# Optimization experiments

Hardware: AMD Instinct MI355X
Metric: run time of the kernel (lower is better)

The kernel has to match this reference:

```python
import jax, jax.numpy as jnp
import numpy as np

B, T, D, H, FF, E = 4, 1024, 1024, 16, 4096, 8
HD = D // H
EPS = 1e-5


def layernorm(x, g, b):
    mu = jnp.mean(x, axis=-1, keepdims=True)
    var = jnp.mean(jnp.square(x - mu), axis=-1, keepdims=True)
    return (x - mu) * jax.lax.rsqrt(var + EPS) * g + b


def setup_inputs() -> dict:
    key = jax.random.key(0)
    ks = jax.random.split(key, 24)
    s = 0.02
    inp = {
        "src": jax.random.normal(ks[0], (B, T, D), jnp.float32),
        "frac": jax.random.uniform(ks[1], (B, T), jnp.float32),
        "Wq": jax.random.normal(ks[2], (D, D), jnp.float32) * s,
        "bq": jnp.zeros((D,), jnp.float32),
        "Wk": jax.random.normal(ks[3], (D, D), jnp.float32) * s,
        "bk": jnp.zeros((D,), jnp.float32),
        "Wv": jax.random.normal(ks[4], (D, D), jnp.float32) * s,
        "bv": jnp.zeros((D,), jnp.float32),
        "Wo": jax.random.normal(ks[5], (D, D), jnp.float32) * s,
        "bo": jnp.zeros((D,), jnp.float32),
        "alpha_pos": jax.random.normal(ks[6], (H,), jnp.float32) * s,
        "alpha_neg": jax.random.normal(ks[7], (H,), jnp.float32) * s,
        "gate_W": jax.random.normal(ks[8], (D, E), jnp.float32) * s,
        "gate_b": jnp.zeros((E,), jnp.float32),
        "W1": jax.random.normal(ks[9], (E, D, FF), jnp.float32) * s,
        "b1": jnp.zeros((E, FF), jnp.float32),
        "W2": jax.random.normal(ks[10], (E, FF, D), jnp.float32) * s,
        "b2": jnp.zeros((E, D), jnp.float32),
        "ln1_g": jnp.ones((D,), jnp.float32),
        "ln1_b": jnp.zeros((D,), jnp.float32),
        "ln2_g": jnp.ones((D,), jnp.float32),
        "ln2_b": jnp.zeros((D,), jnp.float32),
    }
    return inp


def reference(src, frac, Wq, bq, Wk, bk, Wv, bv, Wo, bo, alpha_pos, alpha_neg,
              gate_W, gate_b, W1, b1, W2, b2, ln1_g, ln1_b, ln2_g, ln2_b):
    # ---- attention with per-head stoichiometric bias ----
    q = (src @ Wq + bq).reshape(B, T, H, HD).transpose(0, 2, 1, 3)  # [B,H,T,hd]
    k = (src @ Wk + bk).reshape(B, T, H, HD).transpose(0, 2, 1, 3)
    v = (src @ Wv + bv).reshape(B, T, H, HD).transpose(0, 2, 1, 3)
    scale = HD ** -0.5
    scores = jnp.einsum('bhqd,bhkd->bhqk', q, k) * scale  # [B,H,T,T]
    Dm = frac[:, None, :] - frac[:, :, None]  # frac_j - frac_i, [B,T,T]
    bias = (alpha_pos[None, :, None, None] * jax.nn.relu(Dm)[:, None]
            - alpha_neg[None, :, None, None] * jax.nn.relu(-Dm)[:, None])
    probs = jax.nn.softmax(scores + bias, axis=-1)
    attn = jnp.einsum('bhqk,bhkd->bhqd', probs, v)
    attn = attn.transpose(0, 2, 1, 3).reshape(B, T, D) @ Wo + bo

    x = layernorm(src + attn, ln1_g, ln1_b)

    # ---- top-2 MoE FFN ----
    logits = x @ gate_W + gate_b  # [B,T,E]
    gscores = jax.nn.softmax(logits, axis=-1)
    top2_scores, top2_idx = jax.lax.top_k(gscores, 2)  # [B,T,2]
    # dense per-expert combine weight: score if expert in top-2 else 0
    weights = jnp.sum(jax.nn.one_hot(top2_idx, E, dtype=x.dtype)
                      * top2_scores[..., None], axis=-2)  # [B,T,E]
    ff = jnp.zeros_like(x)
    for e in range(E):  # small fixed expert count
        h = jax.nn.relu(x @ W1[e] + b1[e])
        ff = ff + weights[..., e:e + 1] * (h @ W2[e] + b2[e])

    return layernorm(x + ff, ln2_g, ln2_b)
```

## Files before the change

### kernel.cpp

```cpp
#include <hip/hip_runtime.h>
#include <stdint.h>

typedef unsigned short u16;
typedef unsigned int   u32;

using bf16x8 = __attribute__((ext_vector_type(8))) short;
using f32x4  = __attribute__((ext_vector_type(4))) float;

#define N_T   1024
#define N_D   1024
#define N_E   8
#define N_BT  4096
#define LNEPS 1e-5f

__device__ __forceinline__ u32 rne2(float a, float b) {
  u32 ua = __float_as_uint(a); ua = (ua + 0x7fffu + ((ua >> 16) & 1u)) >> 16;
  u32 ub = __float_as_uint(b); ub = (ub + 0x7fffu + ((ub >> 16) & 1u)) >> 16;
  return ua | (ub << 16);
}
__device__ __forceinline__ u16 rne1(float a) {
  u32 ua = __float_as_uint(a);
  return (u16)((ua + 0x7fffu + ((ua >> 16) & 1u)) >> 16);
}
__device__ __forceinline__ float bfhi_f(float a) {
  u32 ua = __float_as_uint(a);
  ua = (ua + 0x7fffu + ((ua >> 16) & 1u)) & 0xffff0000u;
  return __uint_as_float(ua);
}
__device__ __forceinline__ int fch(int row) { return (row & 3) ^ ((row >> 2) & 3); }
__device__ __forceinline__ int swz(int row, int chunk) {
  return row * 32 + (((chunk ^ fch(row)) & 3) << 3);
}
__device__ __forceinline__ float wred(float v) {
  #pragma unroll
  for (int o2 = 32; o2 > 0; o2 >>= 1) v += __shfl_xor(v, o2, 64);
  return v;
}
__device__ __forceinline__ f32x4 mfma16(bf16x8 a, bf16x8 b, f32x4 c) {
  return __builtin_amdgcn_mfma_f32_16x16x32_bf16(a, b, c, 0, 0, 0);
}
typedef __attribute__((address_space(1))) const u32 gas_u32;
typedef __attribute__((address_space(3))) u32 las_u32;
__device__ __forceinline__ void gl16(const void* g, void* l) {
  __builtin_amdgcn_global_load_lds((gas_u32*)g, (las_u32*)l, 16, 0, 0);
}

template<int SPLIT>
__global__ __launch_bounds__(256)
void transpose_bf16(const float* __restrict__ in, u16* __restrict__ outh,
                    u16* __restrict__ outl, int R, int C, float scale)
{
  __shared__ u16 th[64][68];
  __shared__ u16 tl[SPLIT ? 64 : 1][SPLIT ? 68 : 1];
  const long long zb = (long long)blockIdx.z * R * C;
  const float* srcp = in + zb;
  const int r0 = blockIdx.y * 64, c0 = blockIdx.x * 64;
  const int t = threadIdx.x;
  {
    const int rr = t >> 4, cc = (t & 15) << 2;
    #pragma unroll
    for (int i = 0; i < 4; i++) {
      const int r = rr + i * 16;
      float4 v = *(const float4*)(srcp + (long long)(r0 + r) * C + c0 + cc);
      v.x *= scale; v.y *= scale; v.z *= scale; v.w *= scale;
      if constexpr (SPLIT) {
        float hx = bfhi_f(v.x), hy = bfhi_f(v.y), hz = bfhi_f(v.z), hw = bfhi_f(v.w);
        *(uint2*)&th[r][cc] = make_uint2(rne2(hx, hy), rne2(hz, hw));
        *(uint2*)&tl[r][cc] = make_uint2(rne2(v.x - hx, v.y - hy), rne2(v.z - hz, v.w - hw));
      } else {
        *(uint2*)&th[r][cc] = make_uint2(rne2(v.x, v.y), rne2(v.z, v.w));
      }
    }
  }
  __syncthreads();
  {
    const int c = t >> 2, rs = (t & 3) << 4;
    const long long ob = zb + (long long)(c0 + c) * R + r0 + rs;
    u32 w[8];
    #pragma unroll
    for (int i = 0; i < 8; i++)
      w[i] = (u32)th[rs + 2*i][c] | ((u32)th[rs + 2*i + 1][c] << 16);
    *(uint4*)(outh + ob)     = make_uint4(w[0], w[1], w[2], w[3]);
    *(uint4*)(outh + ob + 8) = make_uint4(w[4], w[5], w[6], w[7]);
    if constexpr (SPLIT) {
      #pragma unroll
      for (int i = 0; i < 8; i++)
        w[i] = (u32)tl[rs + 2*i][c] | ((u32)tl[rs + 2*i + 1][c] << 16);
      *(uint4*)(outl + ob)     = make_uint4(w[0], w[1], w[2], w[3]);
      *(uint4*)(outl + ob + 8) = make_uint4(w[4], w[5], w[6], w[7]);
    }
  }
}

__global__ __launch_bounds__(256)
void trans4(const float* __restrict__ Wq, const float* __restrict__ Wk,
            const float* __restrict__ Wv, const float* __restrict__ Wo,
            u16* __restrict__ Bcath, u16* __restrict__ Bcatl,
            u16* __restrict__ WoTh, u16* __restrict__ WoTl)
{
  __shared__ u16 th[64][68];
  __shared__ u16 tl[64][68];
  const int z = blockIdx.z;
  const float* in = (z == 0) ? Wq : (z == 1) ? Wk : (z == 2) ? Wv : Wo;
  u16* outh = (z == 3) ? WoTh : (Bcath + (long long)z * 1024 * 1024);
  u16* outl = (z == 3) ? WoTl : (Bcatl + (long long)z * 1024 * 1024);
  const float scale = (z == 0) ? 0.125f : 1.0f;
  const int r0 = blockIdx.y * 64, c0 = blockIdx.x * 64;
  const int t = threadIdx.x;
  {
    const int rr = t >> 4, cc = (t & 15) << 2;
    #pragma unroll
    for (int i = 0; i < 4; i++) {
      const int r = rr + i * 16;
      float4 v = *(const float4*)(in + (long long)(r0 + r) * 1024 + c0 + cc);
      v.x *= scale; v.y *= scale; v.z *= scale; v.w *= scale;
      float hx = bfhi_f(v.x), hy = bfhi_f(v.y), hz = bfhi_f(v.z), hw = bfhi_f(v.w);
      *(uint2*)&th[r][cc] = make_uint2(rne2(hx, hy), rne2(hz, hw));
      *(uint2*)&tl[r][cc] = make_uint2(rne2(v.x - hx, v.y - hy), rne2(v.z - hz, v.w - hw));
    }
  }
  __syncthreads();
  {
    const int c = t >> 2, rs = (t & 3) << 4;
    const long long ob = (long long)(c0 + c) * 1024 + r0 + rs;
    u32 w[8];
    #pragma unroll
    for (int i = 0; i < 8; i++)
      w[i] = (u32)th[rs + 2*i][c] | ((u32)th[rs + 2*i + 1][c] << 16);
    *(uint4*)(outh + ob)     = make_uint4(w[0], w[1], w[2], w[3]);
    *(uint4*)(outh + ob + 8) = make_uint4(w[4], w[5], w[6], w[7]);
    #pragma unroll
    for (int i = 0; i < 8; i++)
      w[i] = (u32)tl[rs + 2*i][c] | ((u32)tl[rs + 2*i + 1][c] << 16);
    *(uint4*)(outl + ob)     = make_uint4(w[0], w[1], w[2], w[3]);
    *(uint4*)(outl + ob + 8) = make_uint4(w[4], w[5], w[6], w[7]);
  }
}

__global__ __launch_bounds__(256)
void bias_cat(const float* __restrict__ bq, const float* __restrict__ bk,
              const float* __restrict__ bv, float* __restrict__ bcat)
{
  const int i = blockIdx.x * 256 + threadIdx.x;
  if (i < 1024)       bcat[i] = bq[i] * 0.125f;
  else if (i < 2048)  bcat[i] = bk[i - 1024];
  else if (i < 3072)  bcat[i] = bv[i - 2048];
}

__global__ __launch_bounds__(256)
void vtrans_bf16(const u16* __restrict__ Vh, const u16* __restrict__ Vl, int ldv,
                 u16* __restrict__ Vth, u16* __restrict__ Vtl)
{
  __shared__ u16 th[64][72];
  __shared__ u16 tl[64][72];
  const int bh = blockIdx.y, b = bh >> 4, h = bh & 15;
  const int kt = blockIdx.x, tid = threadIdx.x;
  {
    const int sr = tid >> 2, scb = (tid & 3) << 4;
    const long long off = (long long)(b * N_T + kt * 64 + sr) * ldv + h * 64 + scb;
    const uint4* vh = (const uint4*)(Vh + off);
    const uint4* vl = (const uint4*)(Vl + off);
    *(uint4*)&th[sr][scb]     = vh[0];
    *(uint4*)&th[sr][scb + 8] = vh[1];
    *(uint4*)&tl[sr][scb]     = vl[0];
    *(uint4*)&tl[sr][scb + 8] = vl[1];
  }
  __syncthreads();
  {
    const int od = tid >> 2, os0 = (tid & 3) << 4;
    u16 wh[16], wl[16];
    #pragma unroll
    for (int i = 0; i < 16; i++) { wh[i] = th[os0 + i][od]; wl[i] = tl[os0 + i][od]; }
    u16* oph = Vth + (long long)(bh * 64 + od) * N_T + kt * 64 + os0;
    u16* opl = Vtl + (long long)(bh * 64 + od) * N_T + kt * 64 + os0;
    *(uint4*)oph = make_uint4((u32)wh[0] | ((u32)wh[1] << 16), (u32)wh[2] | ((u32)wh[3] << 16),
                              (u32)wh[4] | ((u32)wh[5] << 16), (u32)wh[6] | ((u32)wh[7] << 16));
    *(uint4*)(oph + 8) = make_uint4((u32)wh[8] | ((u32)wh[9] << 16), (u32)wh[10] | ((u32)wh[11] << 16),
                                    (u32)wh[12] | ((u32)wh[13] << 16), (u32)wh[14] | ((u32)wh[15] << 16));
    *(uint4*)opl = make_uint4((u32)wl[0] | ((u32)wl[1] << 16), (u32)wl[2] | ((u32)wl[3] << 16),
                              (u32)wl[4] | ((u32)wl[5] << 16), (u32)wl[6] | ((u32)wl[7] << 16));
    *(uint4*)(opl + 8) = make_uint4((u32)wl[8] | ((u32)wl[9] << 16), (u32)wl[10] | ((u32)wl[11] << 16),
                                    (u32)wl[12] | ((u32)wl[13] << 16), (u32)wl[14] | ((u32)wl[15] << 16));
  }
}

template<int ASPLIT, int GATHER, int DORELU, int DOSCALE, int OBF, int GROUPED, int CG>
__global__ __launch_bounds__(256, 2)
void gemm128(const void* __restrict__ Ap, int lda,
             const u16* __restrict__ Bhp, const u16* __restrict__ Blp,
             long long bstride,
             void* __restrict__ Cp, int ldc,
             const float* __restrict__ biasp, int bias_stride,
             const float* __restrict__ slot_wp,
             const int* __restrict__ tokidx,
             const int2* __restrict__ tilesp, const int* __restrict__ ntilesp,
             int Ksz, void* __restrict__ Cp2, float cscale)
{
  const int gx = gridDim.x, nwg = gx * gridDim.y;
  const int orig = blockIdx.y * gx + blockIdx.x;
  const int flat = (orig & 7) * (nwg >> 3) + (orig >> 3);
  const int cgsz = gx * CG;
  const int colg = flat / cgsz, rem = flat % cgsz;
  const int bxx = rem / CG;
  const int byy = colg * CG + rem % CG;

  int e = 0, row0;
  if constexpr (GROUPED) {
    if (bxx >= *ntilesp) return;
    const int2 dsc = tilesp[bxx];
    e = dsc.x; row0 = dsc.y;
  } else {
    row0 = bxx * 128;
  }
  const int col0 = byy * 128;

  __shared__ __align__(16) u16 AhS[ASPLIT ? 1 : 3][128 * 32];
  __shared__ __align__(16) u16 BhS[ASPLIT ? 1 : 3][128 * 32];
  __shared__ __align__(16) u16 AlS[ASPLIT ? 128 * 32 : 8];
  __shared__ __align__(16) u16 BlS[ASPLIT ? 128 * 32 : 8];

  const int tid = threadIdx.x, wid = tid >> 6, lane = tid & 63;
  const int wm = (wid >> 1) << 6, wn = (wid & 1) << 6;
  const int l15 = lane & 15, l4 = lane >> 4;

  const int srow0 = wid * 32 + (lane >> 2);
  const int srow1 = srow0 + 16;
  const int sg0 = ((lane & 3) ^ fch(srow0)) << 3;
  const int sg1 = ((lane & 3) ^ fch(srow1)) << 3;
  const int lo0 = wid * 1024, lo1 = wid * 1024 + 512;

  const u16* Bg0 = Bhp + (long long)e * bstride + (long long)(col0 + srow0) * Ksz + sg0;
  const u16* Bg1 = Bhp + (long long)e * bstride + (long long)(col0 + srow1) * Ksz + sg1;
  const u16* Blg0 = nullptr; const u16* Blg1 = nullptr;
  if constexpr (ASPLIT) {
    Blg0 = Blp + (long long)e * bstride + (long long)(col0 + srow0) * Ksz + sg0;
    Blg1 = Blp + (long long)e * bstride + (long long)(col0 + srow1) * Ksz + sg1;
  }

  const u16* Ag0 = nullptr; const u16* Ag1 = nullptr;
  if constexpr (!ASPLIT) {
    long long ar0, ar1;
    if constexpr (GATHER) { ar0 = tokidx[row0 + srow0]; ar1 = tokidx[row0 + srow1]; }
    else                  { ar0 = row0 + srow0;          ar1 = row0 + srow1; }
    Ag0 = (const u16*)Ap + ar0 * (long long)lda + sg0;
    Ag1 = (const u16*)Ap + ar1 * (long long)lda + sg1;
  }

  f32x4 acc[4][4] = {};
  const int nk = Ksz >> 5;

  if constexpr (!ASPLIT) {
    gl16(Ag0, &AhS[0][lo0]); gl16(Ag1, &AhS[0][lo1]);
    gl16(Bg0, &BhS[0][lo0]); gl16(Bg1, &BhS[0][lo1]);
    gl16(Ag0 + 32, &AhS[1][lo0]); gl16(Ag1 + 32, &AhS[1][lo1]);
    gl16(Bg0 + 32, &BhS[1][lo0]); gl16(Bg1 + 32, &BhS[1][lo1]);
    for (int kt = 0; kt < nk; kt++) {
      if (kt + 1 < nk) asm volatile("s_waitcnt vmcnt(4)" ::: "memory");
      else             asm volatile("s_waitcnt vmcnt(0)" ::: "memory");
      __syncthreads();
      const int bi = kt % 3;
      bf16x8 ah[4], bh[4];
      #pragma unroll
      for (int i = 0; i < 4; i++) {
        ah[i] = *(const bf16x8*)&AhS[bi][swz(wm + i * 16 + l15, l4)];
        bh[i] = *(const bf16x8*)&BhS[bi][swz(wn + i * 16 + l15, l4)];
      }
      #pragma unroll
      for (int i = 0; i < 4; i++)
        #pragma unroll
        for (int j = 0; j < 4; j++)
          acc[i][j] = mfma16(ah[i], bh[j], acc[i][j]);
      __syncthreads();
      if (kt + 2 < nk) {
        const int ko = (kt + 2) << 5;
        const int bn = (kt + 2) % 3;
        gl16(Ag0 + ko, &AhS[bn][lo0]);
        gl16(Ag1 + ko, &AhS[bn][lo1]);
        gl16(Bg0 + ko, &BhS[bn][lo0]);
        gl16(Bg1 + ko, &BhS[bn][lo1]);
      }
    }
  } else {
    const int prr = tid >> 1, pc2 = (tid & 1) << 1;
    const float* Arow = (const float*)Ap + (long long)(row0 + prr) * lda;
    uint4 sah0, sah1, sal0, sal1;
    auto gloadA = [&](int k0) {
      const float4* ap = (const float4*)(Arow + k0 + pc2 * 8);
      float4 f0 = ap[0], f1 = ap[1], f2 = ap[2], f3 = ap[3];
      float h0 = bfhi_f(f0.x), h1 = bfhi_f(f0.y), h2 = bfhi_f(f0.z), h3 = bfhi_f(f0.w);
      float h4 = bfhi_f(f1.x), h5 = bfhi_f(f1.y), h6 = bfhi_f(f1.z), h7 = bfhi_f(f1.w);
      sah0 = make_uint4(rne2(h0, h1), rne2(h2, h3), rne2(h4, h5), rne2(h6, h7));
      sal0 = make_uint4(rne2(f0.x - h0, f0.y - h1), rne2(f0.z - h2, f0.w - h3),
                        rne2(f1.x - h4, f1.y - h5), rne2(f1.z - h6, f1.w - h7));
      h0 = bfhi_f(f2.x); h1 = bfhi_f(f2.y); h2 = bfhi_f(f2.z); h3 = bfhi_f(f2.w);
      h4 = bfhi_f(f3.x); h5 = bfhi_f(f3.y); h6 = bfhi_f(f3.z); h7 = bfhi_f(f3.w);
      sah1 = make_uint4(rne2(h0, h1), rne2(h2, h3), rne2(h4, h5), rne2(h6, h7));
      sal1 = make_uint4(rne2(f2.x - h0, f2.y - h1), rne2(f2.z - h2, f2.w - h3),
                        rne2(f3.x - h4, f3.y - h5), rne2(f3.z - h6, f3.w - h7));
    };
    gloadA(0);
    for (int kt = 0; kt < nk; kt++) {
      __syncthreads();
      const int ko = kt << 5;
      *(uint4*)&AhS[0][swz(prr, pc2)]     = sah0;
      *(uint4*)&AhS[0][swz(prr, pc2 + 1)] = sah1;
      *(uint4*)&AlS[swz(prr, pc2)]        = sal0;
      *(uint4*)&AlS[swz(prr, pc2 + 1)]    = sal1;
      gl16(Bg0 + ko, &BhS[0][lo0]);
      gl16(Bg1 + ko, &BhS[0][lo1]);
      gl16(Blg0 + ko, &BlS[lo0]);
      gl16(Blg1 + ko, &BlS[lo1]);
      asm volatile("s_waitcnt vmcnt(0)" ::: "memory");
      __syncthreads();
      if (kt + 1 < nk) gloadA((kt + 1) << 5);

      bf16x8 ah[4], bh[4], al[4], bl[4];
      #pragma unroll
      for (int i = 0; i < 4; i++) {
        const int ar = wm + i * 16 + l15;
        const int br = wn + i * 16 + l15;
        ah[i] = *(const bf16x8*)&AhS[0][swz(ar, l4)];
        bh[i] = *(const bf16x8*)&BhS[0][swz(br, l4)];
        al[i] = *(const bf16x8*)&AlS[swz(ar, l4)];
        bl[i] = *(const bf16x8*)&BlS[swz(br, l4)];
      }
      #pragma unroll
      for (int i = 0; i < 4; i++) {
        #pragma unroll
        for (int j = 0; j < 4; j++) {
          acc[i][j] = mfma16(ah[i], bh[j], acc[i][j]);
          acc[i][j] = mfma16(ah[i], bl[j], acc[i][j]);
          acc[i][j] = mfma16(al[i], bh[j], acc[i][j]);
        }
      }
    }
  }

  #pragma unroll
  for (int i = 0; i < 4; i++) {
    #pragma unroll
    for (int j = 0; j < 4; j++) {
      const int orow0 = row0 + wm + i * 16 + (l4 << 2);
      const int ocol  = col0 + wn + j * 16 + l15;
      const float bv = biasp[(long long)e * bias_stride + col0 + wn + j * 16 + l15];
      #pragma unroll
      for (int q = 0; q < 4; q++) {
        float v = acc[i][j][q] + bv;
        if constexpr (DORELU) v = fmaxf(v, 0.f);
        const long long orow = orow0 + q;
        if constexpr (DOSCALE) v *= slot_wp[orow];
        if constexpr (OBF == 2) {
          const float vs = v * cscale;
          const float hi = bfhi_f(vs);
          ((u16*)Cp )[orow * ldc + ocol] = (u16)(__float_as_uint(hi) >> 16);
          ((u16*)Cp2)[orow * ldc + ocol] = rne1(vs - hi);
        } else if constexpr (OBF == 1) {
          ((u16*)Cp)[orow * ldc + ocol] = rne1(v);
        } else {
          ((float*)Cp)[orow * ldc + ocol] = v;
        }
      }
    }
  }
}

__global__ __launch_bounds__(256, 2)
void attn_mfma(const u16* __restrict__ Qh, const u16* __restrict__ Ql,
               const u16* __restrict__ Kh, const u16* __restrict__ Kl, int ldq,
               const u16* __restrict__ Vth, const u16* __restrict__ Vtl,
               const float* __restrict__ frac,
               const float* __restrict__ apos, const float* __restrict__ aneg,
               float* __restrict__ ctx)
{
  __shared__ __align__(16) u16 KhS[64 * 64];
  __shared__ __align__(16) u16 KlS[64 * 64];
  __shared__ __align__(16) u16 VhS[64 * 64];
  __shared__ __align__(16) u16 VlS[64 * 64];
  __shared__ __align__(16) u16 PS[4][32][72];
  __shared__ __align__(16) float fjS[64];

  const int bh = blockIdx.x, b = bh >> 4, h = bh & 15;
  const int tid = threadIdx.x, wid = tid >> 6, lane = tid & 63;
  const int l15 = lane & 15, l4 = lane >> 4;
  const int q0 = blockIdx.y * 128 + wid * 32;

  bf16x8 qh[2][2], ql[2][2];
  #pragma unroll
  for (int ni = 0; ni < 2; ni++) {
    const long long qoff = (long long)(b * N_T + q0 + ni * 16 + l15) * ldq + h * 64 + l4 * 8;
    #pragma unroll
    for (int ks = 0; ks < 2; ks++) {
      qh[ni][ks] = *(const bf16x8*)(Qh + qoff + ks * 32);
      ql[ni][ks] = *(const bf16x8*)(Ql + qoff + ks * 32);
    }
  }
  float fq[2];
  #pragma unroll
  for (int ni = 0; ni < 2; ni++) fq[ni] = frac[b * N_T + q0 + ni * 16 + l15];
  const float ap = apos[h], an = aneg[h];

  f32x4 acc[4][2] = {};
  float mrun[2] = {-3.0e38f, -3.0e38f}, lrun[2] = {0.f, 0.f};

  const int sr = tid >> 2, scb = (tid & 3) << 4;
  const int ch0 = ((scb >> 3) ^ (sr & 7)) << 3;
  const int ch1 = (((scb >> 3) + 1) ^ (sr & 7)) << 3;

  for (int kt = 0; kt < 16; kt++) {
    __syncthreads();
    {
      const long long koff = (long long)(b * N_T + kt * 64 + sr) * ldq + h * 64 + scb;
      const uint4* khp = (const uint4*)(Kh + koff);
      const uint4* klp = (const uint4*)(Kl + koff);
      const long long voff = (long long)(bh * 64 + sr) * N_T + kt * 64 + scb;
      const uint4* vhp = (const uint4*)(Vth + voff);
      const uint4* vlp = (const uint4*)(Vtl + voff);
      *(uint4*)&KhS[sr * 64 + ch0] = khp[0];
      *(uint4*)&KhS[sr * 64 + ch1] = khp[1];
      *(uint4*)&KlS[sr * 64 + ch0] = klp[0];
      *(uint4*)&KlS[sr * 64 + ch1] = klp[1];
      *(uint4*)&VhS[sr * 64 + ch0] = vhp[0];
      *(uint4*)&VhS[sr * 64 + ch1] = vhp[1];
      *(uint4*)&VlS[sr * 64 + ch0] = vlp[0];
      *(uint4*)&VlS[sr * 64 + ch1] = vlp[1];
    }
    if (tid < 64) fjS[tid] = frac[b * N_T + kt * 64 + tid];
    __syncthreads();

    f32x4 s[4][2] = {};
    #pragma unroll
    for (int ks = 0; ks < 2; ks++) {
      bf16x8 kh[4], kl[4];
      #pragma unroll
      for (int mj = 0; mj < 4; mj++) {
        const int row = mj * 16 + l15;
        const int ch = (((ks << 2) + l4) ^ (row & 7)) << 3;
        kh[mj] = *(const bf16x8*)&KhS[row * 64 + ch];
        kl[mj] = *(const bf16x8*)&KlS[row * 64 + ch];
      }
      #pragma unroll
      for (int mj = 0; mj < 4; mj++) {
        #pragma unroll
        for (int ni = 0; ni < 2; ni++) {
          s[mj][ni] = mfma16(kh[mj], qh[ni][ks], s[mj][ni]);
          s[mj][ni] = mfma16(kh[mj], ql[ni][ks], s[mj][ni]);
          s[mj][ni] = mfma16(kl[mj], qh[ni][ks], s[mj][ni]);
        }
      }
    }

    #pragma unroll
    for (int mj = 0; mj < 4; mj++) {
      const int kvb = mj * 16 + l4 * 4;
      const float f0 = fjS[kvb], f1 = fjS[kvb + 1], f2 = fjS[kvb + 2], f3 = fjS[kvb + 3];
      #pragma unroll
      for (int ni = 0; ni < 2; ni++) {
        float d0 = f0 - fq[ni], d1 = f1 - fq[ni], d2 = f2 - fq[ni], d3 = f3 - fq[ni];
        s[mj][ni][0] += (d0 > 0.f ? ap : an) * d0;
        s[mj][ni][1] += (d1 > 0.f ? ap : an) * d1;
        s[mj][ni][2] += (d2 > 0.f ? ap : an) * d2;
        s[mj][ni][3] += (d3 > 0.f ? ap : an) * d3;
      }
    }

    #pragma unroll
    for (int ni = 0; ni < 2; ni++) {
      float tm = s[0][ni][0];
      #pragma unroll
      for (int mj = 0; mj < 4; mj++) {
        tm = fmaxf(tm, fmaxf(fmaxf(s[mj][ni][0], s[mj][ni][1]),
                             fmaxf(s[mj][ni][2], s[mj][ni][3])));
      }
      tm = fmaxf(tm, __shfl_xor(tm, 16, 64));
      tm = fmaxf(tm, __shfl_xor(tm, 32, 64));
      const float nm = fmaxf(mrun[ni], tm);
      const float cor = __expf(mrun[ni] - nm);
      mrun[ni] = nm;
      lrun[ni] *= cor;
      #pragma unroll
      for (int md = 0; md < 4; md++) {
        acc[md][ni][0] *= cor; acc[md][ni][1] *= cor;
        acc[md][ni][2] *= cor; acc[md][ni][3] *= cor;
      }
      float rsum = 0.f;
      #pragma unroll
      for (int mj = 0; mj < 4; mj++) {
        #pragma unroll
        for (int r = 0; r < 4; r++) {
          const float p = __expf(s[mj][ni][r] - nm);
          s[mj][ni][r] = p;
          rsum += p;
        }
      }
      rsum += __shfl_xor(rsum, 16, 64);
      rsum += __shfl_xor(rsum, 32, 64);
      lrun[ni] += rsum;
    }

    #pragma unroll
    for (int ni = 0; ni < 2; ni++) {
      #pragma unroll
      for (int mj = 0; mj < 4; mj++) {
        float h0 = bfhi_f(s[mj][ni][0]), h1 = bfhi_f(s[mj][ni][1]);
        float h2 = bfhi_f(s[mj][ni][2]), h3 = bfhi_f(s[mj][ni][3]);
        u32* dst = (u32*)&PS[wid][ni * 16 + l15][mj * 16 + l4 * 4];
        dst[0] = rne2(h0, h1); dst[1] = rne2(h2, h3);
      }
    }
    bf16x8 pbh[2][2];
    #pragma unroll
    for (int ni = 0; ni < 2; ni++)
      #pragma unroll
      for (int ks = 0; ks < 2; ks++)
        pbh[ni][ks] = *(const bf16x8*)&PS[wid][ni * 16 + l15][ks * 32 + l4 * 8];

    #pragma unroll
    for (int ni = 0; ni < 2; ni++) {
      #pragma unroll
      for (int mj = 0; mj < 4; mj++) {
        float p0 = s[mj][ni][0], p1 = s[mj][ni][1], p2 = s[mj][ni][2], p3 = s[mj][ni][3];
        float h0 = bfhi_f(p0), h1 = bfhi_f(p1), h2 = bfhi_f(p2), h3 = bfhi_f(p3);
        u32* dst = (u32*)&PS[wid][ni * 16 + l15][mj * 16 + l4 * 4];
        dst[0] = rne2(p0 - h0, p1 - h1); dst[1] = rne2(p2 - h2, p3 - h3);
      }
    }
    bf16x8 pbl[2][2];
    #pragma unroll
    for (int ni = 0; ni < 2; ni++)
      #pragma unroll
      for (int ks = 0; ks < 2; ks++)
        pbl[ni][ks] = *(const bf16x8*)&PS[wid][ni * 16 + l15][ks * 32 + l4 * 8];

    #pragma unroll
    for (int md = 0; md < 4; md++) {
      #pragma unroll
      for (int ks = 0; ks < 2; ks++) {
        const int row = md * 16 + l15;
        const int ch = (((ks << 2) + l4) ^ (row & 7)) << 3;
        const bf16x8 vh = *(const bf16x8*)&VhS[row * 64 + ch];
        const bf16x8 vl = *(const bf16x8*)&VlS[row * 64 + ch];
        #pragma unroll
        for (int nq = 0; nq < 2; nq++) {
          acc[md][nq] = mfma16(vh, pbh[nq][ks], acc[md][nq]);
          acc[md][nq] = mfma16(vh, pbl[nq][ks], acc[md][nq]);
          acc[md][nq] = mfma16(vl, pbh[nq][ks], acc[md][nq]);
        }
      }
    }
  }

  const float inv[2] = {1.f / lrun[0], 1.f / lrun[1]};
  #pragma unroll
  for (int nq = 0; nq < 2; nq++) {
    #pragma unroll
    for (int md = 0; md < 4; md++) {
      float4 o;
      o.x = acc[md][nq][0] * inv[nq];
      o.y = acc[md][nq][1] * inv[nq];
      o.z = acc[md][nq][2] * inv[nq];
      o.w = acc[md][nq][3] * inv[nq];
      *(float4*)(ctx + (long long)(b * N_T + q0 + nq * 16 + l15) * N_D +
                 h * 64 + md * 16 + l4 * 4) = o;
    }
  }
}

__global__ __launch_bounds__(256, 4)
void ln1_gate(const float* __restrict__ src, const float* __restrict__ attnout,
              const float* __restrict__ g, const float* __restrict__ bb,
              const float* __restrict__ gateW, const float* __restrict__ gateb,
              float* __restrict__ xout, u16* __restrict__ xbf,
              int2* __restrict__ tok_top, float2* __restrict__ tok_w)
{
  const int wid = threadIdx.x >> 6, lane = threadIdx.x & 63;
  const int t = blockIdx.x * 4 + wid;
  const float4* s4 = (const float4*)(src + (long long)t * N_D);
  const float4* a4 = (const float4*)(attnout + (long long)t * N_D);
  float4 v[4];
  float sum = 0.f;
  #pragma unroll
  for (int c = 0; c < 4; c++) {
    const int idx = c * 64 + lane;
    float4 a = s4[idx], b2 = a4[idx];
    v[c] = make_float4(a.x + b2.x, a.y + b2.y, a.z + b2.z, a.w + b2.w);
    sum += v[c].x + v[c].y + v[c].z + v[c].w;
  }
  sum = wred(sum);
  const float mu = sum * (1.f / 1024.f);
  float s2 = 0.f;
  #pragma unroll
  for (int c = 0; c < 4; c++) {
    float dx = v[c].x - mu, dy = v[c].y - mu, dz = v[c].z - mu, dw = v[c].w - mu;
    s2 += dx * dx + dy * dy + dz * dz + dw * dw;
  }
  s2 = wred(s2);
  const float rs = rsqrtf(s2 * (1.f / 1024.f) + LNEPS);
  float acc[8];
  #pragma unroll
  for (int e2 = 0; e2 < 8; e2++) acc[e2] = 0.f;
  #pragma unroll
  for (int c = 0; c < 4; c++) {
    const int idx = c * 64 + lane;
    float4 gv = ((const float4*)g)[idx], bv = ((const float4*)bb)[idx];
    float xa[4];
    xa[0] = (v[c].x - mu) * rs * gv.x + bv.x;
    xa[1] = (v[c].y - mu) * rs * gv.y + bv.y;
    xa[2] = (v[c].z - mu) * rs * gv.z + bv.z;
    xa[3] = (v[c].w - mu) * rs * gv.w + bv.w;
    ((float4*)(xout + (long long)t * N_D))[idx] = make_float4(xa[0], xa[1], xa[2], xa[3]);
    *(uint2*)&xbf[(long long)t * N_D + idx * 4] =
        make_uint2(rne2(xa[0], xa[1]), rne2(xa[2], xa[3]));
    #pragma unroll
    for (int ii = 0; ii < 4; ii++) {
      const float xs = xa[ii];
      const float4* gw = (const float4*)(gateW + ((long long)(idx * 4 + ii)) * N_E);
      float4 w0 = gw[0], w1 = gw[1];
      acc[0] += xs * w0.x; acc[1] += xs * w0.y; acc[2] += xs * w0.z; acc[3] += xs * w0.w;
      acc[4] += xs * w1.x; acc[5] += xs * w1.y; acc[6] += xs * w1.z; acc[7] += xs * w1.w;
    }
  }
  #pragma unroll
  for (int e2 = 0; e2 < 8; e2++) acc[e2] = wred(acc[e2]);
  if (lane == 0) {
    float lg[8];
    #pragma unroll
    for (int e2 = 0; e2 < 8; e2++) lg[e2] = acc[e2] + gateb[e2];
    float mx = lg[0];
    #pragma unroll
    for (int e2 = 1; e2 < 8; e2++) mx = fmaxf(mx, lg[e2]);
    float Z = 0.f;
    #pragma unroll
    for (int e2 = 0; e2 < 8; e2++) Z += __expf(lg[e2] - mx);
    int e0 = 0; float v0 = lg[0];
    #pragma unroll
    for (int e2 = 1; e2 < 8; e2++) if (lg[e2] > v0) { v0 = lg[e2]; e0 = e2; }
    int e1 = -1; float v1 = -3.4e38f;
    #pragma unroll
    for (int e2 = 0; e2 < 8; e2++) if (e2 != e0 && lg[e2] > v1) { v1 = lg[e2]; e1 = e2; }
    tok_top[t] = make_int2(e0, e1);
    tok_w[t] = make_float2(__expf(v0 - mx) / Z, __expf(v1 - mx) / Z);
  }
}

__global__ __launch_bounds__(256)
void route_build(const int2* __restrict__ tok_top, int* __restrict__ offsets,
                 int* __restrict__ cursors, int* __restrict__ ntiles,
                 int2* __restrict__ tiles, int* __restrict__ token_idx,
                 float* __restrict__ slot_w)
{
  __shared__ int cnt[N_E];
  __shared__ int soff[N_E + 1];
  __shared__ int scnt[N_E];
  const int tid = threadIdx.x;
  if (tid < N_E) cnt[tid] = 0;
  __syncthreads();
  int lc0 = 0, lc1 = 0, lc2 = 0, lc3 = 0, lc4 = 0, lc5 = 0, lc6 = 0, lc7 = 0;
  for (int t = tid; t < N_BT; t += 256) {
    const int2 ee = tok_top[t];
    lc0 += (ee.x == 0) + (ee.y == 0); lc1 += (ee.x == 1) + (ee.y == 1);
    lc2 += (ee.x == 2) + (ee.y == 2); lc3 += (ee.x == 3) + (ee.y == 3);
    lc4 += (ee.x == 4) + (ee.y == 4); lc5 += (ee.x == 5) + (ee.y == 5);
    lc6 += (ee.x == 6) + (ee.y == 6); lc7 += (ee.x == 7) + (ee.y == 7);
  }
  if (lc0) atomicAdd(&cnt[0], lc0); if (lc1) atomicAdd(&cnt[1], lc1);
  if (lc2) atomicAdd(&cnt[2], lc2); if (lc3) atomicAdd(&cnt[3], lc3);
  if (lc4) atomicAdd(&cnt[4], lc4); if (lc5) atomicAdd(&cnt[5], lc5);
  if (lc6) atomicAdd(&cnt[6], lc6); if (lc7) atomicAdd(&cnt[7], lc7);
  __syncthreads();
  if (tid == 0) {
    int off = 0, nt = 0;
    for (int ex = 0; ex < N_E; ex++) {
      soff[ex] = off; offsets[ex] = off; cursors[ex] = 0;
      const int c = cnt[ex];
      scnt[ex] = c;
      const int pt = (c + 127) >> 7;
      for (int i = 0; i < pt; i++) { tiles[nt] = make_int2(ex, off + i * 128); nt++; }
      off += pt << 7;
    }
    soff[N_E] = off; offsets[N_E] = off;
    *ntiles = nt;
  }
  __syncthreads();
  for (int ex = 0; ex < N_E; ex++)
    for (int s = soff[ex] + scnt[ex] + tid; s < soff[ex + 1]; s += 256) {
      token_idx[s] = 0; slot_w[s] = 0.f;
    }
}

__global__ __launch_bounds__(256)
void route_scatter(const int2* __restrict__ tok_top, const float2* __restrict__ tok_w,
                   const int* __restrict__ offsets, int* __restrict__ cursors,
                   int* __restrict__ token_idx, float* __restrict__ slot_w,
                   int* __restrict__ slotA, int* __restrict__ slotB)
{
  const int t = blockIdx.x * 256 + threadIdx.x;
  if (t >= N_BT) return;
  const int2 ee = tok_top[t];
  const float2 ww = tok_w[t];
  int p = atomicAdd(&cursors[ee.x], 1);
  int s = offsets[ee.x] + p;
  token_idx[s] = t; slot_w[s] = ww.x; slotA[t] = s;
  p = atomicAdd(&cursors[ee.y], 1);
  s = offsets[ee.y] + p;
  token_idx[s] = t; slot_w[s] = ww.y; slotB[t] = s;
}

__global__ __launch_bounds__(256, 4)
void final_ln2(const float* __restrict__ x, const float* __restrict__ out2,
               const int* __restrict__ slotA, const int* __restrict__ slotB,
               const float* __restrict__ g, const float* __restrict__ bb,
               float* __restrict__ out)
{
  const int wid = threadIdx.x >> 6, lane = threadIdx.x & 63;
  const int t = blockIdx.x * 4 + wid;
  const int sA = slotA[t], sB = slotB[t];
  const float4* xr = (const float4*)(x + (long long)t * N_D);
  const float4* pa = (const float4*)(out2 + (long long)sA * N_D);
  const float4* pb = (const float4*)(out2 + (long long)sB * N_D);
  float4 v[4];
  float sum = 0.f;
  #pragma unroll
  for (int c = 0; c < 4; c++) {
    const int idx = c * 64 + lane;
    float4 a = xr[idx], b2 = pa[idx], c2 = pb[idx];
    v[c] = make_float4(a.x + b2.x + c2.x, a.y + b2.y + c2.y,
                       a.z + b2.z + c2.z, a.w + b2.w + c2.w);
    sum += v[c].x + v[c].y + v[c].z + v[c].w;
  }
  sum = wred(sum);
  const float mu = sum * (1.f / 1024.f);
  float s2 = 0.f;
  #pragma unroll
  for (int c = 0; c < 4; c++) {
    float dx = v[c].x - mu, dy = v[c].y - mu, dz = v[c].z - mu, dw = v[c].w - mu;
    s2 += dx * dx + dy * dy + dz * dz + dw * dw;
  }
  s2 = wred(s2);
  const float rs = rsqrtf(s2 * (1.f / 1024.f) + LNEPS);
  #pragma unroll
  for (int c = 0; c < 4; c++) {
    const int idx = c * 64 + lane;
    float4 gv = ((const float4*)g)[idx], bv = ((const float4*)bb)[idx];
    float4 o;
    o.x = (v[c].x - mu) * rs * gv.x + bv.x;
    o.y = (v[c].y - mu) * rs * gv.y + bv.y;
    o.z = (v[c].z - mu) * rs * gv.z + bv.z;
    o.w = (v[c].w - mu) * rs * gv.w + bv.w;
    ((float4*)(out + (long long)t * N_D))[idx] = o;
  }
}

extern "C" void kernel_launch(void* const* d_in, const int* in_sizes, int n_in,
                              void* d_out, int out_size, void* d_ws, size_t ws_size,
                              hipStream_t stream)
{
  const float* src   = (const float*)d_in[0];
  const float* frac  = (const float*)d_in[1];
  const float* Wq    = (const float*)d_in[2];
  const float* bq    = (const float*)d_in[3];
  const float* Wk    = (const float*)d_in[4];
  const float* bk    = (const float*)d_in[5];
  const float* Wv    = (const float*)d_in[6];
  const float* bv    = (const float*)d_in[7];
  const float* Wo    = (const float*)d_in[8];
  const float* bo    = (const float*)d_in[9];
  const float* apos  = (const float*)d_in[10];
  const float* aneg  = (const float*)d_in[11];
  const float* gateW = (const float*)d_in[12];
  const float* gateb = (const float*)d_in[13];
  const float* W1    = (const float*)d_in[14];
  const float* b1    = (const float*)d_in[15];
  const float* W2    = (const float*)d_in[16];
  const float* b2    = (const float*)d_in[17];
  const float* ln1g  = (const float*)d_in[18];
  const float* ln1b  = (const float*)d_in[19];
  const float* ln2g  = (const float*)d_in[20];
  const float* ln2b  = (const float*)d_in[21];
  float* out = (float*)d_out;

  char* ws = (char*)d_ws;
  const size_t MB = 1ull << 20;
  u16* Bcath = (u16*)(ws + 0 * MB);
  u16* Bcatl = (u16*)(ws + 6 * MB);
  u16* WoTh  = (u16*)(ws + 12 * MB);
  u16* WoTl  = (u16*)(ws + 14 * MB);
  u16*   W1T  = (u16*)(ws + 16 * MB);
  float* out2 = (float*)(ws + 16 * MB);
  u16*   W2T  = (u16*)(ws + 80 * MB);
  u16*   QKVh = (u16*)(ws + 144 * MB);
  u16*   QKVl = (u16*)(ws + 168 * MB);
  u16*   Vth  = (u16*)(ws + 192 * MB);
  u16*   Vtl  = (u16*)(ws + 200 * MB);
  float* ctxb = (float*)(ws + 208 * MB);
  float* attnb= (float*)(ws + 144 * MB);
  u16*   hb   = (u16*)(ws + 144 * MB);
  float* xb   = (float*)(ws + 224 * MB);
  u16*   xbf  = (u16*)(ws + 4 * MB);
  float* bcat = (float*)(ws + 240 * MB);
  char* misc = ws + 0;
  int*    cursors   = (int*)(misc + 64);
  int*    offsets   = (int*)(misc + 128);
  int*    ntiles    = (int*)(misc + 256);
  int2*   tiles     = (int2*)(misc + 512);
  int2*   tok_top   = (int2*)(misc + 2048);
  float2* tok_w     = (float2*)(misc + 2048 + 32768);
  int*    token_idx = (int*)(misc + 2048 + 65536);
  float*  slot_w    = (float*)(misc + 2048 + 65536 + 36864);
  int*    slotA     = (int*)(misc + 2048 + 65536 + 73728);
  int*    slotB     = (int*)(misc + 2048 + 65536 + 73728 + 16384);

  dim3 b256(256);
  trans4<<<dim3(16, 16, 4), b256, 0, stream>>>(Wq, Wk, Wv, Wo, Bcath, Bcatl, WoTh, WoTl);
  transpose_bf16<0><<<dim3(64, 16, 8), b256, 0, stream>>>(W1, W1T, nullptr, 1024, 4096, 1.0f);
  transpose_bf16<0><<<dim3(16, 64, 8), b256, 0, stream>>>(W2, W2T, nullptr, 4096, 1024, 1.0f);
  bias_cat<<<dim3(12), b256, 0, stream>>>(bq, bk, bv, bcat);

  gemm128<1, 0, 0, 0, 2, 0, 3><<<dim3(32, 24), b256, 0, stream>>>(
      src, 1024, Bcath, Bcatl, 0, QKVh, 3072, bcat, 0, nullptr, nullptr, nullptr, nullptr,
      1024, QKVl, 1.0f);

  vtrans_bf16<<<dim3(16, 64), b256, 0, stream>>>(QKVh + 2048, QKVl + 2048, 3072, Vth, Vtl);

  attn_mfma<<<dim3(64, 8), b256, 0, stream>>>(QKVh, QKVl, QKVh + 1024, QKVl + 1024, 3072,
                                              Vth, Vtl, frac, apos, aneg, ctxb);

  gemm128<1, 0, 0, 0, 0, 0, 1><<<dim3(32, 8), b256, 0, stream>>>(
      ctxb, 1024, WoTh, WoTl, 0, attnb, 1024, bo, 0, nullptr, nullptr, nullptr, nullptr,
      1024, nullptr, 1.0f);

  ln1_gate<<<dim3(1024), b256, 0, stream>>>(src, attnb, ln1g, ln1b, gateW, gateb,
                                            xb, xbf, tok_top, tok_w);
  route_build<<<dim3(1), b256, 0, stream>>>(tok_top, offsets, cursors, ntiles,
                                            tiles, token_idx, slot_w);
  route_scatter<<<dim3(16), b256, 0, stream>>>(tok_top, tok_w, offsets, cursors,
                                               token_idx, slot_w, slotA, slotB);

  gemm128<0, 1, 1, 0, 1, 1, 4><<<dim3(72, 32), b256, 0, stream>>>(
      xbf, 1024, W1T, nullptr, 4096ll * 1024, hb, 4096, b1, 4096,
      nullptr, token_idx, tiles, ntiles, 1024, nullptr, 1.0f);
  gemm128<0, 0, 0, 1, 0, 1, 8><<<dim3(72, 8), b256, 0, stream>>>(
      hb, 4096, W2T, nullptr, 1024ll * 4096, out2, 1024, b2, 1024,
      slot_w, nullptr, tiles, ntiles, 4096, nullptr, 1.0f);

  final_ln2<<<dim3(1024), b256, 0, stream>>>(xb, out2, slotA, slotB, ln2g, ln2b, out);
}
```

Before: 611.7 us.

## Use double-buffered GEMM pipeline, register-staged B loads, and bf16 MoE output

The non-split GEMM path goes from a three-stage async LDS ring to a double buffer that waits for all loads at the end of every iteration. The split-precision path now loads B through registers alongside A instead of through direct-to-LDS loads. The second expert GEMM writes its output in bf16 (template flag flipped) and final_ln2 unpacks bf16 pairs, halving that intermediate's traffic at some cost in precision. The shallower pipeline risks exposing more memory latency in the main GEMMs.

```diff
diff --git a/kernel.cpp b/kernel.cpp
--- a/kernel.cpp
+++ b/kernel.cpp
@@ -214,8 +214,8 @@
   }
   const int col0 = byy * 128;
 
-  __shared__ __align__(16) u16 AhS[ASPLIT ? 1 : 3][128 * 32];
-  __shared__ __align__(16) u16 BhS[ASPLIT ? 1 : 3][128 * 32];
+  __shared__ __align__(16) u16 AhS[ASPLIT ? 1 : 2][128 * 32];
+  __shared__ __align__(16) u16 BhS[ASPLIT ? 1 : 2][128 * 32];
   __shared__ __align__(16) u16 AlS[ASPLIT ? 128 * 32 : 8];
   __shared__ __align__(16) u16 BlS[ASPLIT ? 128 * 32 : 8];
 
@@ -223,69 +223,60 @@
   const int wm = (wid >> 1) << 6, wn = (wid & 1) << 6;
   const int l15 = lane & 15, l4 = lane >> 4;
 
-  const int srow0 = wid * 32 + (lane >> 2);
-  const int srow1 = srow0 + 16;
-  const int sg0 = ((lane & 3) ^ fch(srow0)) << 3;
-  const int sg1 = ((lane & 3) ^ fch(srow1)) << 3;
-  const int lo0 = wid * 1024, lo1 = wid * 1024 + 512;
-
-  const u16* Bg0 = Bhp + (long long)e * bstride + (long long)(col0 + srow0) * Ksz + sg0;
-  const u16* Bg1 = Bhp + (long long)e * bstride + (long long)(col0 + srow1) * Ksz + sg1;
-  const u16* Blg0 = nullptr; const u16* Blg1 = nullptr;
-  if constexpr (ASPLIT) {
-    Blg0 = Blp + (long long)e * bstride + (long long)(col0 + srow0) * Ksz + sg0;
-    Blg1 = Blp + (long long)e * bstride + (long long)(col0 + srow1) * Ksz + sg1;
-  }
-
-  const u16* Ag0 = nullptr; const u16* Ag1 = nullptr;
+  f32x4 acc[4][4] = {};
+  const int nk = Ksz >> 5;
+
   if constexpr (!ASPLIT) {
+    const int srow0 = wid * 32 + (lane >> 2);
+    const int srow1 = srow0 + 16;
+    const int sg0 = ((lane & 3) ^ fch(srow0)) << 3;
+    const int sg1 = ((lane & 3) ^ fch(srow1)) << 3;
+    const int lo0 = wid * 1024, lo1 = wid * 1024 + 512;
+
+    const u16* Bg0 = Bhp + (long long)e * bstride + (long long)(col0 + srow0) * Ksz + sg0;
+    const u16* Bg1 = Bhp + (long long)e * bstride + (long long)(col0 + srow1) * Ksz + sg1;
     long long ar0, ar1;
     if constexpr (GATHER) { ar0 = tokidx[row0 + srow0]; ar1 = tokidx[row0 + srow1]; }
     else                  { ar0 = row0 + srow0;          ar1 = row0 + srow1; }
-    Ag0 = (const u16*)Ap + ar0 * (long long)lda + sg0;
-    Ag1 = (const u16*)Ap + ar1 * (long long)lda + sg1;
-  }
-
-  f32x4 acc[4][4] = {};
-  const int nk = Ksz >> 5;
-
-  if constexpr (!ASPLIT) {
+    const u16* Ag0 = (const u16*)Ap + ar0 * (long long)lda + sg0;
+    const u16* Ag1 = (const u16*)Ap + ar1 * (long long)lda + sg1;
+
     gl16(Ag0, &AhS[0][lo0]); gl16(Ag1, &AhS[0][lo1]);
     gl16(Bg0, &BhS[0][lo0]); gl16(Bg1, &BhS[0][lo1]);
-    gl16(Ag0 + 32, &AhS[1][lo0]); gl16(Ag1 + 32, &AhS[1][lo1]);
-    gl16(Bg0 + 32, &BhS[1][lo0]); gl16(Bg1 + 32, &BhS[1][lo1]);
+    asm volatile("s_waitcnt vmcnt(0)" ::: "memory");
+    __syncthreads();
+    int cur = 0;
     for (int kt = 0; kt < nk; kt++) {
-      if (kt + 1 < nk) asm volatile("s_waitcnt vmcnt(4)" ::: "memory");
-      else             asm volatile("s_waitcnt vmcnt(0)" ::: "memory");
-      __syncthreads();
-      const int bi = kt % 3;
+      if (kt + 1 < nk) {
+        const int ko = (kt + 1) << 5;
+        gl16(Ag0 + ko, &AhS[cur ^ 1][lo0]);
+        gl16(Ag1 + ko, &AhS[cur ^ 1][lo1]);
+        gl16(Bg0 + ko, &BhS[cur ^ 1][lo0]);
+        gl16(Bg1 + ko, &BhS[cur ^ 1][lo1]);
+      }
       bf16x8 ah[4], bh[4];
       #pragma unroll
       for (int i = 0; i < 4; i++) {
-        ah[i] = *(const bf16x8*)&AhS[bi][swz(wm + i * 16 + l15, l4)];
-        bh[i] = *(const bf16x8*)&BhS[bi][swz(wn + i * 16 + l15, l4)];
+        ah[i] = *(const bf16x8*)&AhS[cur][swz(wm + i * 16 + l15, l4)];
+        bh[i] = *(const bf16x8*)&BhS[cur][swz(wn + i * 16 + l15, l4)];
       }
       #pragma unroll
       for (int i = 0; i < 4; i++)
         #pragma unroll
         for (int j = 0; j < 4; j++)
           acc[i][j] = mfma16(ah[i], bh[j], acc[i][j]);
+      asm volatile("s_waitcnt vmcnt(0)" ::: "memory");
       __syncthreads();
-      if (kt + 2 < nk) {
-        const int ko = (kt + 2) << 5;
-        const int bn = (kt + 2) % 3;
-        gl16(Ag0 + ko, &AhS[bn][lo0]);
-        gl16(Ag1 + ko, &AhS[bn][lo1]);
-        gl16(Bg0 + ko, &BhS[bn][lo0]);
-        gl16(Bg1 + ko, &BhS[bn][lo1]);
-      }
+      cur ^= 1;
     }
   } else {
-    const int prr = tid >> 1, pc2 = (tid & 1) << 1;
-    const float* Arow = (const float*)Ap + (long long)(row0 + prr) * lda;
-    uint4 sah0, sah1, sal0, sal1;
-    auto gloadA = [&](int k0) {
-      const float4* ap = (const float4*)(Arow + k0 + pc2 * 8);
+    const int rr = tid >> 1, c2 = (tid & 1) << 1;
+    const float* Arow = (const float*)Ap + (long long)(row0 + rr) * lda;
+    const u16* Bhrow = Bhp + (long long)e * bstride + (long long)(col0 + rr) * Ksz;
+    const u16* Blrow = Blp + (long long)e * bstride + (long long)(col0 + rr) * Ksz;
+    uint4 sah0, sah1, sal0, sal1, sbh0, sbh1, sbl0, sbl1;
+    auto gload = [&](int k0) {
+      const float4* ap = (const float4*)(Arow + k0 + c2 * 8);
       float4 f0 = ap[0], f1 = ap[1], f2 = ap[2], f3 = ap[3];
       float h0 = bfhi_f(f0.x), h1 = bfhi_f(f0.y), h2 = bfhi_f(f0.z), h3 = bfhi_f(f0.w);
       float h4 = bfhi_f(f1.x), h5 = bfhi_f(f1.y), h6 = bfhi_f(f1.z), h7 = bfhi_f(f1.w);
@@ -297,22 +288,24 @@
       sah1 = make_uint4(rne2(h0, h1), rne2(h2, h3), rne2(h4, h5), rne2(h6, h7));
       sal1 = make_uint4(rne2(f2.x - h0, f2.y - h1), rne2(f2.z - h2, f2.w - h3),
                         rne2(f3.x - h4, f3.y - h5), rne2(f3.z - h6, f3.w - h7));
+      const uint4* bp = (const uint4*)(Bhrow + k0 + c2 * 8);
+      sbh0 = bp[0]; sbh1 = bp[1];
+      const uint4* blp2 = (const uint4*)(Blrow + k0 + c2 * 8);
+      sbl0 = blp2[0]; sbl1 = blp2[1];
     };
-    gloadA(0);
+    gload(0);
     for (int kt = 0; kt < nk; kt++) {
       __syncthreads();
-      const int ko = kt << 5;
-      *(uint4*)&AhS[0][swz(prr, pc2)]     = sah0;
-      *(uint4*)&AhS[0][swz(prr, pc2 + 1)] = sah1;
-      *(uint4*)&AlS[swz(prr, pc2)]        = sal0;
-      *(uint4*)&AlS[swz(prr, pc2 + 1)]    = sal1;
-      gl16(Bg0 + ko, &BhS[0][lo0]);
-      gl16(Bg1 + ko, &BhS[0][lo1]);
-      gl16(Blg0 + ko, &BlS[lo0]);
-      gl16(Blg1 + ko, &BlS[lo1]);
-      asm volatile("s_waitcnt vmcnt(0)" ::: "memory");
+      *(uint4*)&AhS[0][swz(rr, c2)]     = sah0;
+      *(uint4*)&AhS[0][swz(rr, c2 + 1)] = sah1;
+      *(uint4*)&AlS[swz(rr, c2)]        = sal0;
+      *(uint4*)&AlS[swz(rr, c2 + 1)]    = sal1;
+      *(uint4*)&BhS[0][swz(rr, c2)]     = sbh0;
+      *(uint4*)&BhS[0][swz(rr, c2 + 1)] = sbh1;
+      *(uint4*)&BlS[swz(rr, c2)]        = sbl0;
+      *(uint4*)&BlS[swz(rr, c2 + 1)]    = sbl1;
       __syncthreads();
-      if (kt + 1 < nk) gloadA((kt + 1) << 5);
+      if (kt + 1 < nk) gload((kt + 1) << 5);
 
       bf16x8 ah[4], bh[4], al[4], bl[4];
       #pragma unroll
@@ -706,7 +699,7 @@
 }
 
 __global__ __launch_bounds__(256, 4)
-void final_ln2(const float* __restrict__ x, const float* __restrict__ out2,
+void final_ln2(const float* __restrict__ x, const u16* __restrict__ out2,
                const int* __restrict__ slotA, const int* __restrict__ slotB,
                const float* __restrict__ g, const float* __restrict__ bb,
                float* __restrict__ out)
@@ -715,16 +708,21 @@
   const int t = blockIdx.x * 4 + wid;
   const int sA = slotA[t], sB = slotB[t];
   const float4* xr = (const float4*)(x + (long long)t * N_D);
-  const float4* pa = (const float4*)(out2 + (long long)sA * N_D);
-  const float4* pb = (const float4*)(out2 + (long long)sB * N_D);
+  const u16* pa = out2 + (long long)sA * N_D;
+  const u16* pb = out2 + (long long)sB * N_D;
   float4 v[4];
   float sum = 0.f;
   #pragma unroll
   for (int c = 0; c < 4; c++) {
     const int idx = c * 64 + lane;
-    float4 a = xr[idx], b2 = pa[idx], c2 = pb[idx];
-    v[c] = make_float4(a.x + b2.x + c2.x, a.y + b2.y + c2.y,
-                       a.z + b2.z + c2.z, a.w + b2.w + c2.w);
+    float4 a = xr[idx];
+    uint2 ua = *(const uint2*)&pa[idx * 4];
+    uint2 ub = *(const uint2*)&pb[idx * 4];
+    float a0 = __uint_as_float(ua.x << 16), a1 = __uint_as_float(ua.x & 0xffff0000u);
+    float a2 = __uint_as_float(ua.y << 16), a3 = __uint_as_float(ua.y & 0xffff0000u);
+    float b0 = __uint_as_float(ub.x << 16), b1 = __uint_as_float(ub.x & 0xffff0000u);
+    float b2 = __uint_as_float(ub.y << 16), b3 = __uint_as_float(ub.y & 0xffff0000u);
+    v[c] = make_float4(a.x + a0 + b0, a.y + a1 + b1, a.z + a2 + b2, a.w + a3 + b3);
     sum += v[c].x + v[c].y + v[c].z + v[c].w;
   }
   sum = wred(sum);
@@ -785,7 +783,7 @@
   u16* WoTh  = (u16*)(ws + 12 * MB);
   u16* WoTl  = (u16*)(ws + 14 * MB);
   u16*   W1T  = (u16*)(ws + 16 * MB);
-  float* out2 = (float*)(ws + 16 * MB);
+  u16*   out2 = (u16*)(ws + 16 * MB);
   u16*   W2T  = (u16*)(ws + 80 * MB);
   u16*   QKVh = (u16*)(ws + 144 * MB);
   u16*   QKVl = (u16*)(ws + 168 * MB);
@@ -838,7 +836,7 @@
   gemm128<0, 1, 1, 0, 1, 1, 4><<<dim3(72, 32), b256, 0, stream>>>(
       xbf, 1024, W1T, nullptr, 4096ll * 1024, hb, 4096, b1, 4096,
       nullptr, token_idx, tiles, ntiles, 1024, nullptr, 1.0f);
-  gemm128<0, 0, 0, 1, 0, 1, 8><<<dim3(72, 8), b256, 0, stream>>>(
+  gemm128<0, 0, 0, 1, 1, 1, 8><<<dim3(72, 8), b256, 0, stream>>>(
       hb, 4096, W2T, nullptr, 1024ll * 4096, out2, 1024, b2, 1024,
       slot_w, nullptr, tiles, ntiles, 4096, nullptr, 1.0f);
 
```

Result: faster. 581.2 us (-5.0%).
